# Kernel optimization log

Measured on AMD Instinct MI355X. Metric: run time of the kernel, lower is better.

The kernel has to match this reference:

```python
import jax, jax.numpy as jnp
import numpy as np

N = 60000    # total nodes
E = 600000   # total edges
R = 7        # num relations (edge types)
D_IN = 64    # raw node feature dim
D = 128      # hidden_channels
D2 = 64      # hidden_channels // 2
L = 2        # num_layers
EPS = 1e-5   # LayerNorm eps (torch default)


def setup_inputs() -> dict:
    key = jax.random.key(0)
    ks = jax.random.split(key, 10)
    s = 0.05  # xavier-ish scale
    return {
        "x": jax.random.normal(ks[0], (N, D_IN), jnp.float32),
        "edge_index": jax.random.randint(ks[1], (2, E), 0, N, dtype=jnp.int64),
        "edge_type": jax.random.randint(ks[2], (E,), 0, R, dtype=jnp.int64),
        "emb_W": jax.random.normal(ks[3], (D_IN, D), jnp.float32) * s,
        "emb_b": jnp.zeros((D,), jnp.float32),
        "rel_W": jax.random.normal(ks[4], (L, R, D, D), jnp.float32) * s,
        "root_W": jax.random.normal(ks[5], (L, D, D), jnp.float32) * s,
        "conv_b": jnp.zeros((L, D), jnp.float32),
        "ln_g": jnp.ones((L, D), jnp.float32),
        "ln_b": jnp.zeros((L, D), jnp.float32),
        "cls_W1": jax.random.normal(ks[6], (D, D2), jnp.float32) * s,
        "cls_b1": jnp.zeros((D2,), jnp.float32),
        "cls_ln_g": jnp.ones((D2,), jnp.float32),
        "cls_ln_b": jnp.zeros((D2,), jnp.float32),
        "cls_W2": jax.random.normal(ks[7], (D2, 1), jnp.float32) * s,
        "cls_b2": jnp.zeros((1,), jnp.float32),
    }


def _layernorm(h, g, b):
    m = h.mean(-1, keepdims=True)
    v = h.var(-1, keepdims=True)  # population variance, matches torch LayerNorm
    return (h - m) * jax.lax.rsqrt(v + EPS) * g + b


def _rgcn_conv(h, Wrel, Wroot, b, src, dst, edge_type):
    # Transform every node by every relation weight: [R*N, D]
    t = jnp.einsum('nd,rde->rne', h, Wrel).reshape(R * N, D)
    msg = t[edge_type * N + src]                      # [E, D] per-edge messages
    seg = edge_type * N + dst                         # per-(relation, dst) segments
    summed = jax.ops.segment_sum(msg, seg, num_segments=R * N)
    cnt = jax.ops.segment_sum(jnp.ones((E,), msg.dtype), seg, num_segments=R * N)
    mean = summed / jnp.maximum(cnt, 1.0)[:, None]    # scatter-mean per relation
    agg = mean.reshape(R, N, D).sum(0)                # sum over relations
    return agg + h @ Wroot + b


def reference(x, edge_index, edge_type, emb_W, emb_b, rel_W, root_W, conv_b,
              ln_g, ln_b, cls_W1, cls_b1, cls_ln_g, cls_ln_b, cls_W2, cls_b2):
    src, dst = edge_index[0], edge_index[1]
    # Node embedding (features clamped as in original forward)
    h = jnp.clip(x, -10.0, 10.0) @ emb_W + emb_b
    for l in range(L):
        h = _rgcn_conv(h, rel_W[l], root_W[l], conv_b[l], src, dst, edge_type)
        h = jax.nn.relu(_layernorm(h, ln_g[l], ln_b[l]))
        # dropout is identity at inference
    # Classifier on transaction nodes (= all nodes in this unified setup)
    z = jax.nn.relu(_layernorm(h @ cls_W1 + cls_b1, cls_ln_g, cls_ln_b))
    return z @ cls_W2 + cls_b2  # [N, 1] logits
```

## Files before the change

### kernel.cpp

```cpp
#include <hip/hip_runtime.h>
#include <hip/hip_bf16.h>

typedef unsigned int uint;
typedef unsigned short ushort;

#define N_NODES 60000
#define N_EDGES 600000
#define NREL 7
#define D_IN 64
#define DHID 128
#define LEPS 1e-5f
#define EMB_BLKS 938

typedef __attribute__((ext_vector_type(8))) short bf16x8v;
typedef __attribute__((ext_vector_type(4))) float f32x4v;
typedef __attribute__((ext_vector_type(2))) float f32x2v;

#define AS1C(p) ((const __attribute__((address_space(1))) void*)(p))
#define AS3(p)  ((__attribute__((address_space(3))) void*)(p))

__device__ __forceinline__ float bf2f(uint u16) {
    return __uint_as_float(u16 << 16);
}
__device__ __forceinline__ uint f2bf(float f) {
    uint u = __float_as_uint(f);
    uint lsb = (u >> 16) & 1u;
    u += 0x7fffu + lsb;
    return u >> 16;
}
__device__ __forceinline__ uint pack2(float a, float b) {
    return f2bf(a) | (f2bf(b) << 16);
}

__global__ __launch_bounds__(256) void k_prep(const float* __restrict__ relW,
                                              const float* __restrict__ rootW,
                                              const float* __restrict__ embW,
                                              const int* __restrict__ dst,
                                              const int* __restrict__ et,
                                              ushort* __restrict__ Bt,
                                              ushort* __restrict__ Bte,
                                              int* __restrict__ deg8) {
    __shared__ float t[64][65];
    const int tid = threadIdx.x;
    if (blockIdx.x < 64) {
        const int l  = blockIdx.x >> 5;
        const int kt = (blockIdx.x >> 1) & 15;
        const int jt = blockIdx.x & 1;
        #pragma unroll
        for (int i = 0; i < 4; ++i) {
            const int idx = i * 256 + tid;
            const int kr = idx >> 4;
            const int j4 = idx & 15;
            const int kg = kt * 64 + kr;
            const float* src = (kg < 896)
                ? (relW + (size_t)l * 896 * 128 + (size_t)kg * 128)
                : (rootW + (size_t)l * 128 * 128 + (size_t)(kg - 896) * 128);
            const float4 v = *(const float4*)(src + jt * 64 + j4 * 4);
            t[kr][j4 * 4 + 0] = v.x; t[kr][j4 * 4 + 1] = v.y;
            t[kr][j4 * 4 + 2] = v.z; t[kr][j4 * 4 + 3] = v.w;
        }
        __syncthreads();
        uint* btd = (uint*)Bt;
        #pragma unroll
        for (int i = 0; i < 8; ++i) {
            const int idx = i * 256 + tid;
            const int jr = idx >> 5;
            const int kd = idx & 31;
            const uint w = pack2(t[kd * 2][jr], t[kd * 2 + 1][jr]);
            btd[(size_t)l * 65536 + (size_t)(jt * 64 + jr) * 512 + kt * 32 + kd] = w;
        }
    } else if (blockIdx.x < 66) {
        const int jt = blockIdx.x - 64;
        #pragma unroll
        for (int i = 0; i < 4; ++i) {
            const int idx = i * 256 + tid;
            const int kr = idx >> 4;
            const int j4 = idx & 15;
            const float4 v = *(const float4*)(embW + (size_t)kr * 128 + jt * 64 + j4 * 4);
            t[kr][j4 * 4 + 0] = v.x; t[kr][j4 * 4 + 1] = v.y;
            t[kr][j4 * 4 + 2] = v.z; t[kr][j4 * 4 + 3] = v.w;
        }
        __syncthreads();
        uint* btd = (uint*)Bte;
        #pragma unroll
        for (int i = 0; i < 8; ++i) {
            const int idx = i * 256 + tid;
            const int jr = idx >> 5;
            const int kd = idx & 31;
            const uint w = pack2(t[kd * 2][jr], t[kd * 2 + 1][jr]);
            btd[(size_t)(jt * 64 + jr) * 32 + kd] = w;
        }
    } else {
        for (int e = (blockIdx.x - 66) * 256 + tid; e < N_EDGES; e += 1024 * 256)
            atomicAdd(&deg8[dst[e] * 8 + et[e]], 1);
    }
}

__global__ void k_scan1n(const int* __restrict__ deg8, int* __restrict__ rp,
                         int* __restrict__ bsum, int n) {
    __shared__ int s[256];
    const int t = threadIdx.x;
    const int i = blockIdx.x * 256 + t;
    int v = 0;
    if (i < n) {
        const int4 x = *(const int4*)(deg8 + (size_t)i * 8);
        const int4 y = *(const int4*)(deg8 + (size_t)i * 8 + 4);
        v = x.x + x.y + x.z + x.w + y.x + y.y + y.z + y.w;
    }
    s[t] = v;
    __syncthreads();
    for (int o = 1; o < 256; o <<= 1) {
        int uu = (t >= o) ? s[t - o] : 0;
        __syncthreads();
        s[t] += uu;
        __syncthreads();
    }
    if (i < n) rp[i] = s[t] - v;
    if (t == 255) bsum[blockIdx.x] = s[255];
}
__global__ void k_scanmid(int* __restrict__ bs, int nb) {
    __shared__ int s[256];
    __shared__ int carrys;
    const int t = threadIdx.x;
    if (t == 0) carrys = 0;
    __syncthreads();
    const int nch = (nb + 255) / 256;
    for (int ch = 0; ch < nch; ++ch) {
        const int i = ch * 256 + t;
        const int v = (i < nb) ? bs[i] : 0;
        s[t] = v;
        __syncthreads();
        for (int o = 1; o < 256; o <<= 1) {
            int uu = (t >= o) ? s[t - o] : 0;
            __syncthreads();
            s[t] += uu;
            __syncthreads();
        }
        const int carry = carrys;
        if (i < nb) bs[i] = s[t] - v + carry;
        __syncthreads();
        if (t == 255) carrys = carry + s[255];
        __syncthreads();
    }
}
__global__ void k_scanadd(int* __restrict__ a, const int* __restrict__ bsums,
                          int n, int setlast) {
    const int i = blockIdx.x * 256 + threadIdx.x;
    if (i < n) a[i] += bsums[blockIdx.x];
    if (setlast && blockIdx.x == 0 && threadIdx.x == 0) a[n] = N_EDGES;
}

__global__ __launch_bounds__(256) void k_scatemb(const float* __restrict__ x,
                                                 const ushort* __restrict__ Bte,
                                                 const float* __restrict__ ebias,
                                                 ushort* __restrict__ h,
                                                 const int* __restrict__ src,
                                                 const int* __restrict__ dst,
                                                 const int* __restrict__ et,
                                                 const int* __restrict__ rp,
                                                 int* __restrict__ fill,
                                                 uint* __restrict__ csr32) {
    __shared__ alignas(16) ushort sa[64 * 64];
    __shared__ alignas(16) ushort sb[128 * 64];
    const int tid = threadIdx.x;
    if (blockIdx.x >= EMB_BLKS) {
        for (int e = (blockIdx.x - EMB_BLKS) * 256 + tid; e < N_EDGES; e += 1024 * 256) {
            const int d = dst[e];
            const int p = rp[d] + atomicAdd(&fill[d], 1);
            csr32[p] = (uint)src[e] | ((uint)et[e] << 16);
        }
        return;
    }
    const int lane = tid & 63;
    const int wid = tid >> 6;
    const int wrow = wid >> 1, wcol = wid & 1;
    const int l15 = lane & 15, lh = lane >> 4;
    const int row0 = blockIdx.x * 64;

    #pragma unroll
    for (int i = 0; i < 2; ++i) {
        const int p = i * 256 + tid;
        const int row = p >> 3, gq = p & 7;
        const int n = min(row0 + row, N_NODES - 1);
        const float4 xa = *(const float4*)(x + (size_t)n * 64 + gq * 8);
        const float4 xb = *(const float4*)(x + (size_t)n * 64 + gq * 8 + 4);
        uint w[4];
        w[0] = pack2(fminf(fmaxf(xa.x, -10.f), 10.f), fminf(fmaxf(xa.y, -10.f), 10.f));
        w[1] = pack2(fminf(fmaxf(xa.z, -10.f), 10.f), fminf(fmaxf(xa.w, -10.f), 10.f));
        w[2] = pack2(fminf(fmaxf(xb.x, -10.f), 10.f), fminf(fmaxf(xb.y, -10.f), 10.f));
        w[3] = pack2(fminf(fmaxf(xb.z, -10.f), 10.f), fminf(fmaxf(xb.w, -10.f), 10.f));
        *(uint4*)&sa[(row * 8 + (gq ^ (row & 7))) * 8] = make_uint4(w[0], w[1], w[2], w[3]);
    }
    #pragma unroll
    for (int i = 0; i < 4; ++i) {
        const int p = i * 256 + tid;
        const int row = p >> 3, gq = p & 7;
        const uint4 v = *(const uint4*)((const uint*)Bte + (size_t)row * 32 + gq * 4);
        *(uint4*)&sb[(row * 8 + (gq ^ (row & 7))) * 8] = v;
    }
    float bv[4];
    #pragma unroll
    for (int fn = 0; fn < 4; ++fn) bv[fn] = ebias[wcol * 64 + fn * 16 + l15];
    __syncthreads();

    f32x4v acc[2][4];
    #pragma unroll
    for (int fm = 0; fm < 2; ++fm)
        #pragma unroll
        for (int fn = 0; fn < 4; ++fn)
            acc[fm][fn] = (f32x4v){0.f, 0.f, 0.f, 0.f};
    #pragma unroll
    for (int kh = 0; kh < 2; ++kh) {
        bf16x8v af[2], bfr[4];
        #pragma unroll
        for (int fm = 0; fm < 2; ++fm) {
            const int rowa = wrow * 32 + fm * 16 + l15;
            const int slot = (kh * 4 + lh) ^ (rowa & 7);
            af[fm] = *(const bf16x8v*)&sa[rowa * 64 + slot * 8];
        }
        #pragma unroll
        for (int fn = 0; fn < 4; ++fn) {
            const int rowb = wcol * 64 + fn * 16 + l15;
            const int slot = (kh * 4 + lh) ^ (rowb & 7);
            bfr[fn] = *(const bf16x8v*)&sb[rowb * 64 + slot * 8];
        }
        #pragma unroll
        for (int fm = 0; fm < 2; ++fm)
            #pragma unroll
            for (int fn = 0; fn < 4; ++fn)
                acc[fm][fn] = __builtin_amdgcn_mfma_f32_16x16x32_bf16(
                    af[fm], bfr[fn], acc[fm][fn], 0, 0, 0);
    }
    #pragma unroll
    for (int fm = 0; fm < 2; ++fm)
        #pragma unroll
        for (int r = 0; r < 4; ++r) {
            const int row = row0 + wrow * 32 + fm * 16 + lh * 4 + r;
            if (row < N_NODES) {
                #pragma unroll
                for (int fn = 0; fn < 4; ++fn) {
                    const int col = wcol * 64 + fn * 16 + l15;
                    h[(size_t)row * 128 + col] = (ushort)f2bf(acc[fm][fn][r] + bv[fn]);
                }
            }
        }
}

#define ACC2(R, V) do {                                              \
    f32x2v x_;                                                       \
    x_.x = __uint_as_float((V) << 16);                               \
    x_.y = __uint_as_float((V) & 0xFFFF0000u);                       \
    switch (R) {                                                     \
        case 0: a[0] += x_; break;                                   \
        case 1: a[1] += x_; break;                                   \
        case 2: a[2] += x_; break;                                   \
        case 3: a[3] += x_; break;                                   \
        case 4: a[4] += x_; break;                                   \
        case 5: a[5] += x_; break;                                   \
        default: a[6] += x_; break;                                  \
    } } while (0)

__global__ __launch_bounds__(256) void k_agg(const uint* __restrict__ h32,
                                             const int* __restrict__ rp,
                                             const int* __restrict__ cnt8,
                                             const uint* __restrict__ csr32,
                                             uint* __restrict__ M32) {
    const int wave0 = (blockIdx.x * 256 + threadIdx.x) >> 6;
    const int lane = threadIdx.x & 63;
    const int nwaves = gridDim.x * 4;
    if (wave0 >= N_NODES) return;

    int n = wave0;
    int rl = rp[n], rh = rp[n + 1];
    int4 ca = *(const int4*)(cnt8 + (size_t)n * 8);
    int4 cb = *(const int4*)(cnt8 + (size_t)n * 8 + 4);

    while (true) {
        const int n_next = n + nwaves;
        const bool has_next = (n_next < N_NODES);
        int rl_n = 0, rh_n = 0;
        int4 ca_n = {0, 0, 0, 0}, cb_n = {0, 0, 0, 0};
        if (has_next) {
            rl_n = rp[n_next];
            rh_n = rp[n_next + 1];
            ca_n = *(const int4*)(cnt8 + (size_t)n_next * 8);
            cb_n = *(const int4*)(cnt8 + (size_t)n_next * 8 + 4);
        }
        const int beg = __builtin_amdgcn_readfirstlane(rl);
        const int end = __builtin_amdgcn_readfirstlane(rh);
        const int cnt[NREL] = {ca.x, ca.y, ca.z, ca.w, cb.x, cb.y, cb.z};

        f32x2v a[NREL];
        #pragma unroll
        for (int r = 0; r < NREL; ++r) a[r] = (f32x2v){0.f, 0.f};

        #pragma unroll 1
        for (int e = beg; e < end; e += 8) {
            const int4 c0 = *(const int4*)(csr32 + e);
            const int4 c1 = *(const int4*)(csr32 + e + 4);
            int t[8] = {c0.x, c0.y, c0.z, c0.w, c1.x, c1.y, c1.z, c1.w};
            #pragma unroll
            for (int q = 0; q < 8; ++q) t[q] = __builtin_amdgcn_readfirstlane(t[q]);
            uint v[8];
            #pragma unroll
            for (int q = 0; q < 8; ++q)
                if (e + q < end) v[q] = h32[(size_t)(t[q] & 0xFFFF) * 64 + lane];
            #pragma unroll
            for (int q = 0; q < 8; ++q)
                if (e + q < end) ACC2(t[q] >> 16, v[q]);
        }

        const size_t baseN = (size_t)n * 64 + lane;
        #pragma unroll
        for (int r = 0; r < NREL; ++r) {
            const float sc = 1.f / (float)max(cnt[r], 1);
            M32[(size_t)r * (N_NODES * 64) + baseN] = pack2(a[r].x * sc, a[r].y * sc);
        }
        if (!has_next) break;
        n = n_next; rl = rl_n; rh = rh_n; ca = ca_n; cb = cb_n;
    }
}

__global__ __launch_bounds__(512) void k_gemm_mfma(const ushort* __restrict__ A1,
                                                   const ushort* __restrict__ A2,
                                                   const ushort* __restrict__ Bt,
                                                   const float* __restrict__ bias,
                                                   const float* __restrict__ g,
                                                   const float* __restrict__ bb,
                                                   uint* __restrict__ out,
                                                   int nrows) {
    __shared__ alignas(16) union {
        struct { ushort a[2][8192]; ushort b[2][8192]; } s;
        float ep[64 * 132];
    } u;
    __shared__ float sbi[DHID], sg[DHID], sbb[DHID];

    const int tid = threadIdx.x;
    if (tid < DHID) { sbi[tid] = bias[tid]; sg[tid] = g[tid]; sbb[tid] = bb[tid]; }
    const int lane = tid & 63;
    const int wid = tid >> 6;
    const int wrow = wid >> 1;
    const int wcol = wid & 1;
    const int row0 = blockIdx.x * 128;

    int prow[2], pG[2], arow[2];
    #pragma unroll
    for (int hf = 0; hf < 2; ++hf) {
        const int p = hf * 512 + wid * 64 + lane;
        const int r = p >> 3;
        prow[hf] = r;
        pG[hf] = (p & 7) ^ (r & 7);
        arow[hf] = min(row0 + r, nrows - 1);
    }

    auto stage = [&](int buf, int kt) {
        #pragma unroll
        for (int hf = 0; hf < 2; ++hf) {
            const ushort* ga = (kt < 14)
                ? (A1 + ((size_t)(kt >> 1) * N_NODES + arow[hf]) * 128 + (kt & 1) * 64 + pG[hf] * 8)
                : (A2 + (size_t)arow[hf] * 128 + (kt - 14) * 64 + pG[hf] * 8);
            __builtin_amdgcn_global_load_lds(AS1C(ga),
                AS3(&u.s.a[buf][(hf * 512 + wid * 64) * 8]), 16, 0, 0);
            const ushort* gb = Bt + (size_t)prow[hf] * 1024 + kt * 64 + pG[hf] * 8;
            __builtin_amdgcn_global_load_lds(AS1C(gb),
                AS3(&u.s.b[buf][(hf * 512 + wid * 64) * 8]), 16, 0, 0);
        }
    };

    f32x4v acc[2][4];
    #pragma unroll
    for (int fm = 0; fm < 2; ++fm)
        #pragma unroll
        for (int fn = 0; fn < 4; ++fn)
            acc[fm][fn] = (f32x4v){0.f, 0.f, 0.f, 0.f};

    auto compute = [&](int buf) {
        #pragma unroll
        for (int kh = 0; kh < 2; ++kh) {
            bf16x8v af[2], bfr[4];
            #pragma unroll
            for (int fm = 0; fm < 2; ++fm) {
                const int rowa = wrow * 32 + fm * 16 + (lane & 15);
                const int sa = (kh * 4 + (lane >> 4)) ^ (rowa & 7);
                af[fm] = *(const bf16x8v*)&u.s.a[buf][rowa * 64 + sa * 8];
            }
            #pragma unroll
            for (int fn = 0; fn < 4; ++fn) {
                const int rowb = wcol * 64 + fn * 16 + (lane & 15);
                const int sb = (kh * 4 + (lane >> 4)) ^ (rowb & 7);
                bfr[fn] = *(const bf16x8v*)&u.s.b[buf][rowb * 64 + sb * 8];
            }
            #pragma unroll
            for (int fm = 0; fm < 2; ++fm)
                #pragma unroll
                for (int fn = 0; fn < 4; ++fn)
                    acc[fm][fn] = __builtin_amdgcn_mfma_f32_16x16x32_bf16(
                        af[fm], bfr[fn], acc[fm][fn], 0, 0, 0);
        }
    };

    stage(0, 0);
    #pragma unroll 1
    for (int kt = 0; kt < 16; ++kt) {
        const int cur = kt & 1;
        if (kt < 15) {
            stage(cur ^ 1, kt + 1);
            asm volatile("s_waitcnt vmcnt(4)\n\ts_barrier" ::: "memory");
        } else {
            asm volatile("s_waitcnt vmcnt(0)\n\ts_barrier" ::: "memory");
        }
        compute(cur);
        asm volatile("s_barrier" ::: "memory");
    }
    __syncthreads();

    const int hw = wrow >> 1;
    #pragma unroll 1
    for (int hh = 0; hh < 2; ++hh) {
        if (hw == hh) {
            #pragma unroll
            for (int fm = 0; fm < 2; ++fm) {
                const int rl = (wrow & 1) * 32 + fm * 16 + (lane >> 4) * 4;
                #pragma unroll
                for (int fn = 0; fn < 4; ++fn) {
                    const int cl = wcol * 64 + fn * 16 + (lane & 15);
                    const float bi = sbi[cl];
                    #pragma unroll
                    for (int r = 0; r < 4; ++r)
                        u.ep[(rl + r) * 132 + cl] = acc[fm][fn][r] + bi;
                }
            }
        }
        __syncthreads();
        {
            const int r_loc = tid >> 3, cb = tid & 7;
            const int row_g = row0 + hh * 64 + r_loc;
            float v[16];
            float s = 0.f, sq = 0.f;
            #pragma unroll
            for (int q = 0; q < 4; ++q) {
                const float4 t4 = *(const float4*)&u.ep[r_loc * 132 + cb * 16 + q * 4];
                v[4 * q + 0] = t4.x; v[4 * q + 1] = t4.y;
                v[4 * q + 2] = t4.z; v[4 * q + 3] = t4.w;
                s += t4.x + t4.y + t4.z + t4.w;
                sq += t4.x * t4.x + t4.y * t4.y + t4.z * t4.z + t4.w * t4.w;
            }
            s += __shfl_xor(s, 1, 64); sq += __shfl_xor(sq, 1, 64);
            s += __shfl_xor(s, 2, 64); sq += __shfl_xor(sq, 2, 64);
            s += __shfl_xor(s, 4, 64); sq += __shfl_xor(sq, 4, 64);
            const float mean = s * (1.f / 128.f);
            const float var = sq * (1.f / 128.f) - mean * mean;
            const float rs = rsqrtf(var + LEPS);
            if (row_g < nrows) {
                uint o[8];
                #pragma unroll
                for (int q2 = 0; q2 < 8; ++q2) {
                    const int c0 = cb * 16 + 2 * q2;
                    const float va = fmaxf((v[2 * q2]     - mean) * rs * sg[c0]     + sbb[c0],     0.f);
                    const float vb = fmaxf((v[2 * q2 + 1] - mean) * rs * sg[c0 + 1] + sbb[c0 + 1], 0.f);
                    o[q2] = pack2(va, vb);
                }
                uint* op = out + (size_t)row_g * 64 + cb * 8;
                *(uint4*)(op + 0) = make_uint4(o[0], o[1], o[2], o[3]);
                *(uint4*)(op + 4) = make_uint4(o[4], o[5], o[6], o[7]);
            }
        }
        __syncthreads();
    }
}

__global__ __launch_bounds__(256) void k_cls(const ushort* __restrict__ h16,
                                             const float* __restrict__ W1,
                                             const float* __restrict__ b1,
                                             const float* __restrict__ lg,
                                             const float* __restrict__ lb,
                                             const float* __restrict__ W2,
                                             const float* __restrict__ b2,
                                             float* __restrict__ outp, int nrows) {
    __shared__ ushort Bs[16 * 64 * 8];
    const int tid = threadIdx.x;
    #pragma unroll
    for (int i = 0; i < 8; ++i) {
        const int q = i * 256 + tid;
        const int k = q >> 4;
        const int j0 = (q & 15) * 4;
        const float4 w = *(const float4*)(W1 + (size_t)k * 64 + j0);
        const int gg = k >> 3, kp = k & 7;
        const int jx = (gg & 3) << 4;
        Bs[(gg * 64 + ((j0 + 0) ^ jx)) * 8 + kp] = (ushort)f2bf(w.x);
        Bs[(gg * 64 + ((j0 + 1) ^ jx)) * 8 + kp] = (ushort)f2bf(w.y);
        Bs[(gg * 64 + ((j0 + 2) ^ jx)) * 8 + kp] = (ushort)f2bf(w.z);
        Bs[(gg * 64 + ((j0 + 3) ^ jx)) * 8 + kp] = (ushort)f2bf(w.w);
    }
    const int lane = tid & 63, wid = tid >> 6;
    const int l15 = lane & 15, lh = lane >> 4;
    float lgv[4], lbv[4], w2v[4], b1v[4];
    #pragma unroll
    for (int fn = 0; fn < 4; ++fn) {
        const int col = fn * 16 + l15;
        lgv[fn] = lg[col]; lbv[fn] = lb[col]; w2v[fn] = W2[col]; b1v[fn] = b1[col];
    }
    const float b2v = b2[0];
    __syncthreads();

    const int row0 = blockIdx.x * 128;
    f32x4v acc[2][4];
    #pragma unroll
    for (int fm = 0; fm < 2; ++fm)
        #pragma unroll
        for (int fn = 0; fn < 4; ++fn)
            acc[fm][fn] = (f32x4v){0.f, 0.f, 0.f, 0.f};

    #pragma unroll
    for (int kk = 0; kk < 4; ++kk) {
        bf16x8v af[2], bfr[4];
        #pragma unroll
        for (int fm = 0; fm < 2; ++fm) {
            const int row = min(row0 + wid * 32 + fm * 16 + l15, nrows - 1);
            af[fm] = *(const bf16x8v*)(h16 + (size_t)row * 128 + kk * 32 + lh * 8);
        }
        #pragma unroll
        for (int fn = 0; fn < 4; ++fn) {
            const int gg = kk * 4 + lh;
            const int jc = fn * 16 + l15;
            bfr[fn] = *(const bf16x8v*)&Bs[(gg * 64 + (jc ^ ((gg & 3) << 4))) * 8];
        }
        #pragma unroll
        for (int fm = 0; fm < 2; ++fm)
            #pragma unroll
            for (int fn = 0; fn < 4; ++fn)
                acc[fm][fn] = __builtin_amdgcn_mfma_f32_16x16x32_bf16(
                    af[fm], bfr[fn], acc[fm][fn], 0, 0, 0);
    }

    #pragma unroll
    for (int fm = 0; fm < 2; ++fm)
        #pragma unroll
        for (int r = 0; r < 4; ++r) {
            float cv[4];
            float s = 0.f, sq = 0.f;
            #pragma unroll
            for (int fn = 0; fn < 4; ++fn) {
                cv[fn] = acc[fm][fn][r] + b1v[fn];
                s += cv[fn]; sq += cv[fn] * cv[fn];
            }
            s += __shfl_xor(s, 1, 64); sq += __shfl_xor(sq, 1, 64);
            s += __shfl_xor(s, 2, 64); sq += __shfl_xor(sq, 2, 64);
            s += __shfl_xor(s, 4, 64); sq += __shfl_xor(sq, 4, 64);
            s += __shfl_xor(s, 8, 64); sq += __shfl_xor(sq, 8, 64);
            const float mean = s * (1.f / 64.f);
            const float var = sq * (1.f / 64.f) - mean * mean;
            const float rs = rsqrtf(var + LEPS);
            float dot = 0.f;
            #pragma unroll
            for (int fn = 0; fn < 4; ++fn)
                dot += fmaxf((cv[fn] - mean) * rs * lgv[fn] + lbv[fn], 0.f) * w2v[fn];
            dot += __shfl_xor(dot, 1, 64);
            dot += __shfl_xor(dot, 2, 64);
            dot += __shfl_xor(dot, 4, 64);
            dot += __shfl_xor(dot, 8, 64);
            const int row = row0 + wid * 32 + fm * 16 + lh * 4 + r;
            if (l15 == 0 && row < nrows) outp[row] = dot + b2v;
        }
}

extern "C" void kernel_launch(void* const* d_in, const int* in_sizes, int n_in,
                              void* d_out, int out_size, void* d_ws, size_t ws_size,
                              hipStream_t stream) {
    const float* x      = (const float*)d_in[0];
    const int*   eidx   = (const int*)d_in[1];
    const int*   etype  = (const int*)d_in[2];
    const float* emb_W  = (const float*)d_in[3];
    const float* emb_b  = (const float*)d_in[4];
    const float* rel_W  = (const float*)d_in[5];
    const float* root_W = (const float*)d_in[6];
    const float* conv_b = (const float*)d_in[7];
    const float* ln_g   = (const float*)d_in[8];
    const float* ln_b   = (const float*)d_in[9];
    const float* cls_W1 = (const float*)d_in[10];
    const float* cls_b1 = (const float*)d_in[11];
    const float* cls_lg = (const float*)d_in[12];
    const float* cls_lb = (const float*)d_in[13];
    const float* cls_W2 = (const float*)d_in[14];
    const float* cls_b2 = (const float*)d_in[15];

    const int* srcv = eidx;
    const int* dstv = eidx + N_EDGES;

    char* ws = (char*)d_ws;
    size_t off = 0;
    auto alloc = [&](size_t bytes) { void* p = ws + off; off += (bytes + 255) & ~(size_t)255; return p; };
    uint*   h0    = (uint*)alloc((size_t)N_NODES * 64 * 4);
    uint*   h1    = (uint*)alloc((size_t)N_NODES * 64 * 4);
    uint*   M     = (uint*)alloc((size_t)NREL * N_NODES * 64 * 4);
    int*    rp    = (int*)alloc((size_t)(N_NODES + 1) * 4);
    int*    cnts  = (int*)alloc((size_t)(N_NODES * 9) * 4);
    uint*   csr32 = (uint*)alloc((size_t)N_EDGES * 4);
    ushort* Btb   = (ushort*)alloc((size_t)2 * 128 * 1024 * 2);
    ushort* Bte   = (ushort*)alloc((size_t)128 * 64 * 2);
    int*    bs    = (int*)alloc(4096);
    int*    deg8  = cnts;
    int*    fill  = cnts + N_NODES * 8;
    (void)ws_size; (void)n_in; (void)in_sizes; (void)out_size;

    const int SB = (N_NODES + 255) / 256;
    const int GEMM_BLKS = (N_NODES + 127) / 128;

    hipMemsetAsync(cnts, 0, (size_t)(N_NODES * 9) * 4, stream);
    k_prep<<<66 + 1024, 256, 0, stream>>>(rel_W, root_W, emb_W, dstv, etype,
                                          Btb, Bte, deg8);
    k_scan1n<<<SB, 256, 0, stream>>>(deg8, rp, bs, N_NODES);
    k_scanmid<<<1, 256, 0, stream>>>(bs, SB);
    k_scanadd<<<SB, 256, 0, stream>>>(rp, bs, N_NODES, 1);
    k_scatemb<<<EMB_BLKS + 1024, 256, 0, stream>>>(x, Bte, emb_b, (ushort*)h0,
                                                   srcv, dstv, etype, rp, fill, csr32);

    for (int l = 0; l < 2; ++l) {
        const uint* hin = l ? h1 : h0;
        uint* hout = l ? h0 : h1;
        k_agg<<<2048, 256, 0, stream>>>(hin, rp, deg8, csr32, M);
        k_gemm_mfma<<<GEMM_BLKS, 512, 0, stream>>>(
            (const ushort*)M, (const ushort*)hin,
            Btb + (size_t)l * 131072,
            conv_b + l * 128, ln_g + l * 128, ln_b + l * 128,
            hout, N_NODES);
    }
    k_cls<<<469, 256, 0, stream>>>((const ushort*)h0, cls_W1, cls_b1, cls_lg, cls_lb,
                                   cls_W2, cls_b2, (float*)d_out, N_NODES);
}
```

Measured before the change: 235.1 us.

## Transform nodes per relation first, then gather weighted messages with fused LayerNorm

Replaces aggregate-then-GEMM with transform-then-gather. A batched MFMA kernel first computes all eight per-relation and root transforms of h into a T buffer. A per-node gather kernel then sums per-edge messages weighted by precomputed 1/deg, adds the root term and bias, and applies LayerNorm and ReLU in registers. This removes the large M intermediate round trip and the 16-step K-loop GEMM, and uses one accumulator instead of seven per relation. In exchange it writes a slightly larger T buffer and gathers from it rather than from the much smaller h, which may hurt cache locality.

New measurement: 228.2 us. 1.03x faster.

```diff
diff --git a/kernel.cpp b/kernel.cpp
--- a/kernel.cpp
+++ b/kernel.cpp
@@ -14,7 +14,6 @@
 
 typedef __attribute__((ext_vector_type(8))) short bf16x8v;
 typedef __attribute__((ext_vector_type(4))) float f32x4v;
-typedef __attribute__((ext_vector_type(2))) float f32x2v;
 
 #define AS1C(p) ((const __attribute__((address_space(1))) void*)(p))
 #define AS3(p)  ((__attribute__((address_space(3))) void*)(p))
@@ -37,37 +36,39 @@
                                               const float* __restrict__ embW,
                                               const int* __restrict__ dst,
                                               const int* __restrict__ et,
-                                              ushort* __restrict__ Bt,
+                                              ushort* __restrict__ Btr,
                                               ushort* __restrict__ Bte,
                                               int* __restrict__ deg8) {
     __shared__ float t[64][65];
     const int tid = threadIdx.x;
     if (blockIdx.x < 64) {
         const int l  = blockIdx.x >> 5;
-        const int kt = (blockIdx.x >> 1) & 15;
-        const int jt = blockIdx.x & 1;
+        const int b5 = blockIdx.x & 31;
+        const int r  = b5 >> 2;
+        const int kt = (b5 >> 1) & 1;
+        const int jt = b5 & 1;
         #pragma unroll
         for (int i = 0; i < 4; ++i) {
             const int idx = i * 256 + tid;
             const int kr = idx >> 4;
             const int j4 = idx & 15;
             const int kg = kt * 64 + kr;
-            const float* src = (kg < 896)
-                ? (relW + (size_t)l * 896 * 128 + (size_t)kg * 128)
-                : (rootW + (size_t)l * 128 * 128 + (size_t)(kg - 896) * 128);
-            const float4 v = *(const float4*)(src + jt * 64 + j4 * 4);
+            const float* src = (r < 7)
+                ? (relW + (((size_t)l * 7 + r) * 128 + kg) * 128 + jt * 64 + j4 * 4)
+                : (rootW + ((size_t)l * 128 + kg) * 128 + jt * 64 + j4 * 4);
+            const float4 v = *(const float4*)src;
             t[kr][j4 * 4 + 0] = v.x; t[kr][j4 * 4 + 1] = v.y;
             t[kr][j4 * 4 + 2] = v.z; t[kr][j4 * 4 + 3] = v.w;
         }
         __syncthreads();
-        uint* btd = (uint*)Bt;
+        uint* btd = (uint*)Btr;
         #pragma unroll
         for (int i = 0; i < 8; ++i) {
             const int idx = i * 256 + tid;
             const int jr = idx >> 5;
             const int kd = idx & 31;
             const uint w = pack2(t[kd * 2][jr], t[kd * 2 + 1][jr]);
-            btd[(size_t)l * 65536 + (size_t)(jt * 64 + jr) * 512 + kt * 32 + kd] = w;
+            btd[((size_t)(l * 8 + r) * 128 + jt * 64 + jr) * 64 + kt * 32 + kd] = w;
         }
     } else if (blockIdx.x < 66) {
         const int jt = blockIdx.x - 64;
@@ -158,16 +159,20 @@
                                                  const int* __restrict__ dst,
                                                  const int* __restrict__ et,
                                                  const int* __restrict__ rp,
+                                                 const int* __restrict__ deg8,
                                                  int* __restrict__ fill,
-                                                 uint* __restrict__ csr32) {
+                                                 uint* __restrict__ csr32,
+                                                 float* __restrict__ w32) {
     __shared__ alignas(16) ushort sa[64 * 64];
     __shared__ alignas(16) ushort sb[128 * 64];
     const int tid = threadIdx.x;
     if (blockIdx.x >= EMB_BLKS) {
         for (int e = (blockIdx.x - EMB_BLKS) * 256 + tid; e < N_EDGES; e += 1024 * 256) {
             const int d = dst[e];
+            const int r = et[e];
             const int p = rp[d] + atomicAdd(&fill[d], 1);
-            csr32[p] = (uint)src[e] | ((uint)et[e] << 16);
+            csr32[p] = (uint)(r * N_NODES + src[e]);
+            w32[p] = 1.0f / (float)deg8[d * 8 + r];
         }
         return;
     }
@@ -246,102 +251,19 @@
         }
 }
 
-#define ACC2(R, V) do {                                              \
-    f32x2v x_;                                                       \
-    x_.x = __uint_as_float((V) << 16);                               \
-    x_.y = __uint_as_float((V) & 0xFFFF0000u);                       \
-    switch (R) {                                                     \
-        case 0: a[0] += x_; break;                                   \
-        case 1: a[1] += x_; break;                                   \
-        case 2: a[2] += x_; break;                                   \
-        case 3: a[3] += x_; break;                                   \
-        case 4: a[4] += x_; break;                                   \
-        case 5: a[5] += x_; break;                                   \
-        default: a[6] += x_; break;                                  \
-    } } while (0)
-
-__global__ __launch_bounds__(256) void k_agg(const uint* __restrict__ h32,
-                                             const int* __restrict__ rp,
-                                             const int* __restrict__ cnt8,
-                                             const uint* __restrict__ csr32,
-                                             uint* __restrict__ M32) {
-    const int wave0 = (blockIdx.x * 256 + threadIdx.x) >> 6;
-    const int lane = threadIdx.x & 63;
-    const int nwaves = gridDim.x * 4;
-    if (wave0 >= N_NODES) return;
-
-    int n = wave0;
-    int rl = rp[n], rh = rp[n + 1];
-    int4 ca = *(const int4*)(cnt8 + (size_t)n * 8);
-    int4 cb = *(const int4*)(cnt8 + (size_t)n * 8 + 4);
-
-    while (true) {
-        const int n_next = n + nwaves;
-        const bool has_next = (n_next < N_NODES);
-        int rl_n = 0, rh_n = 0;
-        int4 ca_n = {0, 0, 0, 0}, cb_n = {0, 0, 0, 0};
-        if (has_next) {
-            rl_n = rp[n_next];
-            rh_n = rp[n_next + 1];
-            ca_n = *(const int4*)(cnt8 + (size_t)n_next * 8);
-            cb_n = *(const int4*)(cnt8 + (size_t)n_next * 8 + 4);
-        }
-        const int beg = __builtin_amdgcn_readfirstlane(rl);
-        const int end = __builtin_amdgcn_readfirstlane(rh);
-        const int cnt[NREL] = {ca.x, ca.y, ca.z, ca.w, cb.x, cb.y, cb.z};
-
-        f32x2v a[NREL];
-        #pragma unroll
-        for (int r = 0; r < NREL; ++r) a[r] = (f32x2v){0.f, 0.f};
-
-        #pragma unroll 1
-        for (int e = beg; e < end; e += 8) {
-            const int4 c0 = *(const int4*)(csr32 + e);
-            const int4 c1 = *(const int4*)(csr32 + e + 4);
-            int t[8] = {c0.x, c0.y, c0.z, c0.w, c1.x, c1.y, c1.z, c1.w};
-            #pragma unroll
-            for (int q = 0; q < 8; ++q) t[q] = __builtin_amdgcn_readfirstlane(t[q]);
-            uint v[8];
-            #pragma unroll
-            for (int q = 0; q < 8; ++q)
-                if (e + q < end) v[q] = h32[(size_t)(t[q] & 0xFFFF) * 64 + lane];
-            #pragma unroll
-            for (int q = 0; q < 8; ++q)
-                if (e + q < end) ACC2(t[q] >> 16, v[q]);
-        }
-
-        const size_t baseN = (size_t)n * 64 + lane;
-        #pragma unroll
-        for (int r = 0; r < NREL; ++r) {
-            const float sc = 1.f / (float)max(cnt[r], 1);
-            M32[(size_t)r * (N_NODES * 64) + baseN] = pack2(a[r].x * sc, a[r].y * sc);
-        }
-        if (!has_next) break;
-        n = n_next; rl = rl_n; rh = rh_n; ca = ca_n; cb = cb_n;
-    }
-}
-
-__global__ __launch_bounds__(512) void k_gemm_mfma(const ushort* __restrict__ A1,
-                                                   const ushort* __restrict__ A2,
-                                                   const ushort* __restrict__ Bt,
-                                                   const float* __restrict__ bias,
-                                                   const float* __restrict__ g,
-                                                   const float* __restrict__ bb,
-                                                   uint* __restrict__ out,
-                                                   int nrows) {
-    __shared__ alignas(16) union {
-        struct { ushort a[2][8192]; ushort b[2][8192]; } s;
-        float ep[64 * 132];
-    } u;
-    __shared__ float sbi[DHID], sg[DHID], sbb[DHID];
-
+__global__ __launch_bounds__(512) void k_trans(const ushort* __restrict__ h16,
+                                               const ushort* __restrict__ Btr,
+                                               ushort* __restrict__ T16,
+                                               int nrows) {
+    __shared__ alignas(16) ushort sa[2][8192];
+    __shared__ alignas(16) ushort sb[2][8192];
     const int tid = threadIdx.x;
-    if (tid < DHID) { sbi[tid] = bias[tid]; sg[tid] = g[tid]; sbb[tid] = bb[tid]; }
     const int lane = tid & 63;
     const int wid = tid >> 6;
-    const int wrow = wid >> 1;
-    const int wcol = wid & 1;
+    const int wrow = wid >> 1, wcol = wid & 1;
+    const int l15 = lane & 15, lh = lane >> 4;
     const int row0 = blockIdx.x * 128;
+    const int bj = blockIdx.y;
 
     int prow[2], pG[2], arow[2];
     #pragma unroll
@@ -352,20 +274,19 @@
         pG[hf] = (p & 7) ^ (r & 7);
         arow[hf] = min(row0 + r, nrows - 1);
     }
-
-    auto stage = [&](int buf, int kt) {
+    #pragma unroll
+    for (int kt = 0; kt < 2; ++kt) {
         #pragma unroll
         for (int hf = 0; hf < 2; ++hf) {
-            const ushort* ga = (kt < 14)
-                ? (A1 + ((size_t)(kt >> 1) * N_NODES + arow[hf]) * 128 + (kt & 1) * 64 + pG[hf] * 8)
-                : (A2 + (size_t)arow[hf] * 128 + (kt - 14) * 64 + pG[hf] * 8);
+            const ushort* ga = h16 + (size_t)arow[hf] * 128 + kt * 64 + pG[hf] * 8;
             __builtin_amdgcn_global_load_lds(AS1C(ga),
-                AS3(&u.s.a[buf][(hf * 512 + wid * 64) * 8]), 16, 0, 0);
-            const ushort* gb = Bt + (size_t)prow[hf] * 1024 + kt * 64 + pG[hf] * 8;
+                AS3(&sa[kt][(hf * 512 + wid * 64) * 8]), 16, 0, 0);
+            const ushort* gb = Btr + ((size_t)bj * 128 + prow[hf]) * 128 + kt * 64 + pG[hf] * 8;
             __builtin_amdgcn_global_load_lds(AS1C(gb),
-                AS3(&u.s.b[buf][(hf * 512 + wid * 64) * 8]), 16, 0, 0);
-        }
-    };
+                AS3(&sb[kt][(hf * 512 + wid * 64) * 8]), 16, 0, 0);
+        }
+    }
+    __syncthreads();
 
     f32x4v acc[2][4];
     #pragma unroll
@@ -374,21 +295,22 @@
         for (int fn = 0; fn < 4; ++fn)
             acc[fm][fn] = (f32x4v){0.f, 0.f, 0.f, 0.f};
 
-    auto compute = [&](int buf) {
+    #pragma unroll
+    for (int kt = 0; kt < 2; ++kt)
         #pragma unroll
         for (int kh = 0; kh < 2; ++kh) {
             bf16x8v af[2], bfr[4];
             #pragma unroll
             for (int fm = 0; fm < 2; ++fm) {
-                const int rowa = wrow * 32 + fm * 16 + (lane & 15);
-                const int sa = (kh * 4 + (lane >> 4)) ^ (rowa & 7);
-                af[fm] = *(const bf16x8v*)&u.s.a[buf][rowa * 64 + sa * 8];
+                const int rowa = wrow * 32 + fm * 16 + l15;
+                const int slot = (kh * 4 + lh) ^ (rowa & 7);
+                af[fm] = *(const bf16x8v*)&sa[kt][rowa * 64 + slot * 8];
             }
             #pragma unroll
             for (int fn = 0; fn < 4; ++fn) {
-                const int rowb = wcol * 64 + fn * 16 + (lane & 15);
-                const int sb = (kh * 4 + (lane >> 4)) ^ (rowb & 7);
-                bfr[fn] = *(const bf16x8v*)&u.s.b[buf][rowb * 64 + sb * 8];
+                const int rowb = wcol * 64 + fn * 16 + l15;
+                const int slot = (kh * 4 + lh) ^ (rowb & 7);
+                bfr[fn] = *(const bf16x8v*)&sb[kt][rowb * 64 + slot * 8];
             }
             #pragma unroll
             for (int fm = 0; fm < 2; ++fm)
@@ -397,75 +319,77 @@
                     acc[fm][fn] = __builtin_amdgcn_mfma_f32_16x16x32_bf16(
                         af[fm], bfr[fn], acc[fm][fn], 0, 0, 0);
         }
-    };
-
-    stage(0, 0);
+
+    #pragma unroll
+    for (int fm = 0; fm < 2; ++fm)
+        #pragma unroll
+        for (int r = 0; r < 4; ++r) {
+            const int row = row0 + wrow * 32 + fm * 16 + lh * 4 + r;
+            if (row < nrows) {
+                ushort* tp = T16 + ((size_t)bj * N_NODES + row) * 128 + wcol * 64 + l15;
+                #pragma unroll
+                for (int fn = 0; fn < 4; ++fn)
+                    tp[fn * 16] = (ushort)f2bf(acc[fm][fn][r]);
+            }
+        }
+}
+
+__global__ __launch_bounds__(256) void k_gather(const uint* __restrict__ T32,
+                                                const int* __restrict__ rp,
+                                                const uint* __restrict__ csr32,
+                                                const float* __restrict__ w32,
+                                                const float* __restrict__ bias,
+                                                const float* __restrict__ g,
+                                                const float* __restrict__ bb,
+                                                uint* __restrict__ hout) {
+    const int wave = (blockIdx.x * 256 + threadIdx.x) >> 6;
+    const int lane = threadIdx.x & 63;
+    const int nwaves = gridDim.x * 4;
+    const float2 bias2 = *(const float2*)(bias + 2 * lane);
+    const float2 g2 = *(const float2*)(g + 2 * lane);
+    const float2 b2 = *(const float2*)(bb + 2 * lane);
     #pragma unroll 1
-    for (int kt = 0; kt < 16; ++kt) {
-        const int cur = kt & 1;
-        if (kt < 15) {
-            stage(cur ^ 1, kt + 1);
-            asm volatile("s_waitcnt vmcnt(4)\n\ts_barrier" ::: "memory");
-        } else {
-            asm volatile("s_waitcnt vmcnt(0)\n\ts_barrier" ::: "memory");
-        }
-        compute(cur);
-        asm volatile("s_barrier" ::: "memory");
-    }
-    __syncthreads();
-
-    const int hw = wrow >> 1;
-    #pragma unroll 1
-    for (int hh = 0; hh < 2; ++hh) {
-        if (hw == hh) {
-            #pragma unroll
-            for (int fm = 0; fm < 2; ++fm) {
-                const int rl = (wrow & 1) * 32 + fm * 16 + (lane >> 4) * 4;
-                #pragma unroll
-                for (int fn = 0; fn < 4; ++fn) {
-                    const int cl = wcol * 64 + fn * 16 + (lane & 15);
-                    const float bi = sbi[cl];
-                    #pragma unroll
-                    for (int r = 0; r < 4; ++r)
-                        u.ep[(rl + r) * 132 + cl] = acc[fm][fn][r] + bi;
+    for (int n0 = wave; n0 < N_NODES; n0 += nwaves) {
+        const int n = __builtin_amdgcn_readfirstlane(n0);
+        const int beg = __builtin_amdgcn_readfirstlane(rp[n]);
+        const int end = __builtin_amdgcn_readfirstlane(rp[n + 1]);
+        float ax = 0.f, ay = 0.f;
+        #pragma unroll 1
+        for (int e = beg; e < end; e += 8) {
+            const int4 c0 = *(const int4*)(csr32 + e);
+            const int4 c1 = *(const int4*)(csr32 + e + 4);
+            const float4 w0 = *(const float4*)(w32 + e);
+            const float4 w1 = *(const float4*)(w32 + e + 4);
+            int t[8] = {c0.x, c0.y, c0.z, c0.w, c1.x, c1.y, c1.z, c1.w};
+            const float w[8] = {w0.x, w0.y, w0.z, w0.w, w1.x, w1.y, w1.z, w1.w};
+            #pragma unroll
+            for (int q = 0; q < 8; ++q) t[q] = __builtin_amdgcn_readfirstlane(t[q]);
+            uint v[8];
+            #pragma unroll
+            for (int q = 0; q < 8; ++q)
+                if (e + q < end) v[q] = T32[(size_t)t[q] * 64 + lane];
+            #pragma unroll
+            for (int q = 0; q < 8; ++q)
+                if (e + q < end) {
+                    ax += w[q] * __uint_as_float(v[q] << 16);
+                    ay += w[q] * __uint_as_float(v[q] & 0xFFFF0000u);
                 }
-            }
-        }
-        __syncthreads();
-        {
-            const int r_loc = tid >> 3, cb = tid & 7;
-            const int row_g = row0 + hh * 64 + r_loc;
-            float v[16];
-            float s = 0.f, sq = 0.f;
-            #pragma unroll
-            for (int q = 0; q < 4; ++q) {
-                const float4 t4 = *(const float4*)&u.ep[r_loc * 132 + cb * 16 + q * 4];
-                v[4 * q + 0] = t4.x; v[4 * q + 1] = t4.y;
-                v[4 * q + 2] = t4.z; v[4 * q + 3] = t4.w;
-                s += t4.x + t4.y + t4.z + t4.w;
-                sq += t4.x * t4.x + t4.y * t4.y + t4.z * t4.z + t4.w * t4.w;
-            }
-            s += __shfl_xor(s, 1, 64); sq += __shfl_xor(sq, 1, 64);
-            s += __shfl_xor(s, 2, 64); sq += __shfl_xor(sq, 2, 64);
-            s += __shfl_xor(s, 4, 64); sq += __shfl_xor(sq, 4, 64);
-            const float mean = s * (1.f / 128.f);
-            const float var = sq * (1.f / 128.f) - mean * mean;
-            const float rs = rsqrtf(var + LEPS);
-            if (row_g < nrows) {
-                uint o[8];
-                #pragma unroll
-                for (int q2 = 0; q2 < 8; ++q2) {
-                    const int c0 = cb * 16 + 2 * q2;
-                    const float va = fmaxf((v[2 * q2]     - mean) * rs * sg[c0]     + sbb[c0],     0.f);
-                    const float vb = fmaxf((v[2 * q2 + 1] - mean) * rs * sg[c0 + 1] + sbb[c0 + 1], 0.f);
-                    o[q2] = pack2(va, vb);
-                }
-                uint* op = out + (size_t)row_g * 64 + cb * 8;
-                *(uint4*)(op + 0) = make_uint4(o[0], o[1], o[2], o[3]);
-                *(uint4*)(op + 4) = make_uint4(o[4], o[5], o[6], o[7]);
-            }
-        }
-        __syncthreads();
+        }
+        const uint vr = T32[((size_t)7 * N_NODES + n) * 64 + lane];
+        const float c0f = ax + bf2f(vr & 0xFFFFu) + bias2.x;
+        const float c1f = ay + bf2f(vr >> 16) + bias2.y;
+        float s = c0f + c1f, sq = c0f * c0f + c1f * c1f;
+        #pragma unroll
+        for (int o = 1; o < 64; o <<= 1) {
+            s += __shfl_xor(s, o, 64);
+            sq += __shfl_xor(sq, o, 64);
+        }
+        const float mean = s * (1.f / 128.f);
+        const float var = sq * (1.f / 128.f) - mean * mean;
+        const float rs = rsqrtf(var + LEPS);
+        const float y0 = fmaxf((c0f - mean) * rs * g2.x + b2.x, 0.f);
+        const float y1 = fmaxf((c1f - mean) * rs * g2.y + b2.y, 0.f);
+        hout[(size_t)n * 64 + lane] = pack2(y0, y1);
     }
 }
 
@@ -590,13 +514,13 @@
     char* ws = (char*)d_ws;
     size_t off = 0;
     auto alloc = [&](size_t bytes) { void* p = ws + off; off += (bytes + 255) & ~(size_t)255; return p; };
-    uint*   h0    = (uint*)alloc((size_t)N_NODES * 64 * 4);
-    uint*   h1    = (uint*)alloc((size_t)N_NODES * 64 * 4);
-    uint*   M     = (uint*)alloc((size_t)NREL * N_NODES * 64 * 4);
+    ushort* h     = (ushort*)alloc((size_t)N_NODES * 128 * 2);
+    ushort* T     = (ushort*)alloc((size_t)8 * N_NODES * 128 * 2);
     int*    rp    = (int*)alloc((size_t)(N_NODES + 1) * 4);
     int*    cnts  = (int*)alloc((size_t)(N_NODES * 9) * 4);
     uint*   csr32 = (uint*)alloc((size_t)N_EDGES * 4);
-    ushort* Btb   = (ushort*)alloc((size_t)2 * 128 * 1024 * 2);
+    float*  w32   = (float*)alloc((size_t)N_EDGES * 4);
+    ushort* Btr   = (ushort*)alloc((size_t)2 * 8 * 128 * 128 * 2);
     ushort* Bte   = (ushort*)alloc((size_t)128 * 64 * 2);
     int*    bs    = (int*)alloc(4096);
     int*    deg8  = cnts;
@@ -604,27 +528,26 @@
     (void)ws_size; (void)n_in; (void)in_sizes; (void)out_size;
 
     const int SB = (N_NODES + 255) / 256;
-    const int GEMM_BLKS = (N_NODES + 127) / 128;
+    const int ROW_BLKS = (N_NODES + 127) / 128;
 
     hipMemsetAsync(cnts, 0, (size_t)(N_NODES * 9) * 4, stream);
     k_prep<<<66 + 1024, 256, 0, stream>>>(rel_W, root_W, emb_W, dstv, etype,
-                                          Btb, Bte, deg8);
+                                          Btr, Bte, deg8);
     k_scan1n<<<SB, 256, 0, stream>>>(deg8, rp, bs, N_NODES);
     k_scanmid<<<1, 256, 0, stream>>>(bs, SB);
     k_scanadd<<<SB, 256, 0, stream>>>(rp, bs, N_NODES, 1);
-    k_scatemb<<<EMB_BLKS + 1024, 256, 0, stream>>>(x, Bte, emb_b, (ushort*)h0,
-                                                   srcv, dstv, etype, rp, fill, csr32);
+    k_scatemb<<<EMB_BLKS + 1024, 256, 0, stream>>>(x, Bte, emb_b, h,
+                                                   srcv, dstv, etype, rp, deg8,
+                                                   fill, csr32, w32);
 
     for (int l = 0; l < 2; ++l) {
-        const uint* hin = l ? h1 : h0;
-        uint* hout = l ? h0 : h1;
-        k_agg<<<2048, 256, 0, stream>>>(hin, rp, deg8, csr32, M);
-        k_gemm_mfma<<<GEMM_BLKS, 512, 0, stream>>>(
-            (const ushort*)M, (const ushort*)hin,
-            Btb + (size_t)l * 131072,
+        k_trans<<<dim3(ROW_BLKS, 8), 512, 0, stream>>>(
+            h, Btr + (size_t)l * 131072, T, N_NODES);
+        k_gather<<<2048, 256, 0, stream>>>(
+            (const uint*)T, rp, csr32, w32,
             conv_b + l * 128, ln_g + l * 128, ln_b + l * 128,
-            hout, N_NODES);
-    }
-    k_cls<<<469, 256, 0, stream>>>((const ushort*)h0, cls_W1, cls_b1, cls_lg, cls_lb,
+            (uint*)h);
+    }
+    k_cls<<<469, 256, 0, stream>>>(h, cls_W1, cls_b1, cls_lg, cls_lb,
                                    cls_W2, cls_b2, (float*)d_out, N_NODES);
 }
```
